# Optimization experiments

Hardware: AMD Instinct MI355X
Metric: run time of the kernel (lower is better)

The kernel has to match this reference:

```python
import jax, jax.numpy as jnp
import numpy as np

T, N, F = 32, 100000, 2
E = 1600000
H4 = 4 * F  # PyTorch LSTM packs gates i,f,g,o


def setup_inputs() -> dict:
    key = jax.random.key(0)
    ks = jax.random.split(key, 8)
    stdv = 1.0 / np.sqrt(F)
    x = jax.random.normal(ks[0], (T, N, F), dtype=jnp.float32)
    edge_index = jax.random.randint(ks[1], (2, E), 0, N, dtype=jnp.int32)
    mask = jax.random.randint(ks[2], (N,), 0, 2, dtype=jnp.int32).astype(bool)
    labels = jnp.zeros((N,), dtype=jnp.int32)
    edge_weight = jnp.ones((E,), dtype=jnp.float32)
    data = 0  # unused placeholder (pyg Data object in original)
    w_ih = jax.random.uniform(ks[3], (H4, F), minval=-stdv, maxval=stdv, dtype=jnp.float32)
    w_hh = jax.random.uniform(ks[4], (H4, F), minval=-stdv, maxval=stdv, dtype=jnp.float32)
    b_ih = jax.random.uniform(ks[5], (H4,), minval=-stdv, maxval=stdv, dtype=jnp.float32)
    b_hh = jax.random.uniform(ks[6], (H4,), minval=-stdv, maxval=stdv, dtype=jnp.float32)
    return {"x": x, "edge_index": edge_index, "mask": mask, "labels": labels,
            "edge_weight": edge_weight, "data": data,
            "w_ih": w_ih, "w_hh": w_hh, "b_ih": b_ih, "b_hh": b_hh}


def _interpolate(x, src, dst, n_nodes):
    # Iteratively fill zero entries with the mean over neighbors whose node
    # has any nonzero data (matches A[row_no_data,:]=0 edge filtering).
    def cond(carry):
        xx, i = carry
        return jnp.logical_and(jnp.any(xx == 0), i < 20)

    def body(carry):
        xx, i = carry
        has_data = jnp.sum(xx != 0, axis=(0, 2)) > 0            # [N]
        valid = has_data[src].astype(xx.dtype)                   # [E]
        msg = xx[:, src, :] * valid[None, :, None]               # [T,E,F]
        agg = jax.ops.segment_sum(jnp.transpose(msg, (1, 0, 2)), dst,
                                  num_segments=n_nodes)          # [N,T,F]
        cnt = jax.ops.segment_sum(valid, dst, num_segments=n_nodes)  # [N]
        mean = jnp.transpose(agg, (1, 0, 2)) / jnp.where(cnt > 0, cnt, 1.0)[None, :, None]
        return jnp.where(xx == 0, mean, xx), i + 1

    out, _ = jax.lax.while_loop(cond, body, (x, jnp.int32(0)))
    return out


def _lstm(x_seq, w_ih, w_hh, b_ih, b_hh):
    # x_seq: [T, N, F]; single-layer LSTM, hidden size F, gate order i,f,g,o.
    n, h = x_seq.shape[1], w_hh.shape[1]
    def step(carry, xt):
        hp, cp = carry
        g = xt @ w_ih.T + b_ih + hp @ w_hh.T + b_hh              # [N, 4F]
        i_, f_, g_, o_ = jnp.split(g, 4, axis=-1)
        i_ = jax.nn.sigmoid(i_); f_ = jax.nn.sigmoid(f_)
        g_ = jnp.tanh(g_);        o_ = jax.nn.sigmoid(o_)
        c = f_ * cp + i_ * g_
        hh = o_ * jnp.tanh(c)
        return (hh, c), hh
    z = jnp.zeros((n, h), dtype=x_seq.dtype)
    _, out = jax.lax.scan(step, (z, z), x_seq)
    return out


def reference(x, edge_index, mask, labels, edge_weight, data, w_ih, w_hh, b_ih, b_hh):
    masked = jnp.where(mask[None, :, None], x, jnp.zeros((), x.dtype))
    src, dst = edge_index[0], edge_index[1]
    interp_x = _interpolate(masked, src, dst, x.shape[1])
    return _lstm(interp_x, w_ih, w_hh, b_ih, b_hh)
```

## Files before the change

kernel.cpp:

```cpp
#include <hip/hip_runtime.h>
#include <math.h>

#define TT    32
#define NN    100000
#define FF    2
#define ROW   64
#define EE    1600000
#define MAXIT 20
#define LDSROW 66
#define BIGIT (1 << 29)
#define NR    8
#define RNG   (NN / NR)
#define SLOT  28
#define SLAB  (2 * SLOT)

typedef float f32x4 __attribute__((ext_vector_type(4)));
typedef float f32x2 __attribute__((ext_vector_type(2)));

__device__ __forceinline__ float fsig(float x) { return 1.0f / (1.0f + __expf(-x)); }
__device__ __forceinline__ float ftanh(float x) { return 2.0f / (1.0f + __expf(-2.0f * x)) - 1.0f; }

__global__ void k_mt_flags(const float* __restrict__ x, const int* __restrict__ mask,
                           float* __restrict__ xx, int* __restrict__ fill_iter,
                           unsigned char* __restrict__ hz, unsigned char* __restrict__ hd,
                           int* __restrict__ cnt_v, int* __restrict__ cnt_i,
                           int* __restrict__ wl_count) {
    __shared__ float tile[64 * LDSROW];
    const int n0 = blockIdx.x * 64;
    const int tid = threadIdx.x;

    if (tid < 64 && n0 + tid < NN) { cnt_v[n0 + tid] = 0; cnt_i[n0 + tid] = 0; }
    if (blockIdx.x == 0 && tid < 32) wl_count[tid] = 0;

#pragma unroll
    for (int r = 0; r < 16; r++) {
        int flat = r * 256 + tid;
        int t = flat >> 7;
        int col = flat & 127;
        int gcol = n0 * 2 + col;
        if (gcol < NN * FF) {
            int n = n0 + (col >> 1);
            float v = __builtin_nontemporal_load(x + (size_t)t * (NN * FF) + gcol);
            v = mask[n] ? v : 0.0f;
            tile[(col >> 1) * LDSROW + t * 2 + (col & 1)] = v;
        }
    }
    __syncthreads();

    const int lane = tid & 63, w = tid >> 6;
    for (int i = 0; i < 16; i++) {
        int ln = w * 16 + i;
        int n = n0 + ln;
        if (n >= NN) break;
        float v = tile[ln * LDSROW + lane];
        unsigned long long nzm = __ballot(v != 0.0f);
        if (lane == 0) {
            fill_iter[n] = (nzm != 0ull) ? 0 : BIGIT;
            hz[n] = (nzm != ~0ull) ? 1 : 0;
            hd[n] = (nzm != 0ull) ? 1 : 0;
        }
    }

#pragma unroll
    for (int j = 0; j < 4; j++) {
        int flat4 = j * 256 + tid;
        int ln = flat4 >> 4;
        int n = n0 + ln;
        if (n >= NN) continue;
        int off = (flat4 & 15) * 4;
        float4 v;
        v.x = tile[ln * LDSROW + off + 0];
        v.y = tile[ln * LDSROW + off + 1];
        v.z = tile[ln * LDSROW + off + 2];
        v.w = tile[ln * LDSROW + off + 3];
        *(float4*)(xx + (size_t)n * ROW + off) = v;
    }
}

__global__ void k_fill_slots(const int* __restrict__ ei, const unsigned char* __restrict__ hz,
                             const unsigned char* __restrict__ hd,
                             int* __restrict__ cnt_v, int* __restrict__ cnt_i,
                             int* __restrict__ slab) {
    const int r = blockIdx.x & (NR - 1);
    const int lo = r * RNG, hi = lo + RNG;
    const int gid = (blockIdx.x >> 3) * blockDim.x + threadIdx.x;
    const int stride = (gridDim.x >> 3) * blockDim.x;
    for (int e = gid; e < EE; e += stride) {
        int dst = ei[EE + e];
        if (dst < lo || dst >= hi) continue;
        if (!hz[dst]) continue;
        int src = ei[e];
        if (hd[src]) {
            int pos = atomicAdd(&cnt_v[dst], 1);
            if (pos < SLOT) slab[dst * SLAB + pos] = src;
        } else {
            int pos = atomicAdd(&cnt_i[dst], 1);
            if (pos < SLOT) slab[dst * SLAB + SLOT + pos] = src;
        }
    }
}

__device__ __forceinline__ void gather_node4(int n, int k, int lane,
                                             int vbeg, int vend, int ibeg, int iend,
                                             const int* __restrict__ slab,
                                             int* __restrict__ fill_iter,
                                             float* __restrict__ xx,
                                             int* __restrict__ wl_next,
                                             int* __restrict__ wl_count) {
    const int g = lane >> 4;
    const int s = lane & 15;
    float ax = 0.f, ay = 0.f, az = 0.f, aw = 0.f, cntv = 0.f;
#pragma unroll 2
    for (int e = vbeg + g; e < vend; e += 4) {
        int src = slab[e];
        f32x4 v = ((const f32x4*)(xx + (size_t)src * ROW))[s];
        ax += v.x; ay += v.y; az += v.z; aw += v.w; cntv += 1.f;
    }
    for (int e = ibeg + g; e < iend; e += 4) {
        int src = slab[e];
        if (fill_iter[src] < k) {
            f32x4 v = ((const f32x4*)(xx + (size_t)src * ROW))[s];
            ax += v.x; ay += v.y; az += v.z; aw += v.w; cntv += 1.f;
        }
    }
#pragma unroll
    for (int d = 16; d <= 32; d <<= 1) {
        ax += __shfl_xor(ax, d, 64);
        ay += __shfl_xor(ay, d, 64);
        az += __shfl_xor(az, d, 64);
        aw += __shfl_xor(aw, d, 64);
        cntv += __shfl_xor(cntv, d, 64);
    }
    f32x4 own = ((const f32x4*)(xx + (size_t)n * ROW))[s];
    bool has = cntv > 0.f;
    f32x4 nv;
    nv.x = (own.x == 0.f && has) ? ax / cntv : own.x;
    nv.y = (own.y == 0.f && has) ? ay / cntv : own.y;
    nv.z = (own.z == 0.f && has) ? az / cntv : own.z;
    nv.w = (own.w == 0.f && has) ? aw / cntv : own.w;
    bool allnz = (nv.x != 0.f) & (nv.y != 0.f) & (nv.z != 0.f) & (nv.w != 0.f);
    bool anynz = (nv.x != 0.f) | (nv.y != 0.f) | (nv.z != 0.f) | (nv.w != 0.f);
    unsigned long long ba = __ballot(allnz);
    unsigned long long bn = __ballot(anynz);
    if (g == 0) ((f32x4*)(xx + (size_t)n * ROW))[s] = nv;
    if (lane == 0) {
        if (bn != 0ull && fill_iter[n] > k) fill_iter[n] = k;
        if (ba != ~0ull) {
            int pos = atomicAdd(&wl_count[k], 1);
            wl_next[pos] = n;
        }
    }
}

__global__ void k_gather_first(const unsigned char* __restrict__ hz,
                               const int* __restrict__ cnt_v, const int* __restrict__ slab,
                               int* __restrict__ fill_iter, float* __restrict__ xx,
                               int* __restrict__ wl_next, int* __restrict__ wl_count) {
    const int lane = threadIdx.x & 63;
    int wave = (blockIdx.x * blockDim.x + threadIdx.x) >> 6;
    const int nwaves = (gridDim.x * blockDim.x) >> 6;
    for (int n0 = wave; n0 < NN; n0 += nwaves) {
        int n = __builtin_amdgcn_readfirstlane(n0);
        if (!hz[n]) continue;
        int cv = cnt_v[n]; if (cv > SLOT) cv = SLOT;
        gather_node4(n, 1, lane, n * SLAB, n * SLAB + cv, 0, 0,
                     slab, fill_iter, xx, wl_next, wl_count);
    }
}

__global__ __launch_bounds__(1024)
void k_gather_rest(int* __restrict__ wl_a, int* __restrict__ wl_b,
                   int* __restrict__ wl_count,
                   const int* __restrict__ cnt_v, const int* __restrict__ cnt_i,
                   const int* __restrict__ slab,
                   int* __restrict__ fill_iter, float* __restrict__ xx) {
    const int lane = threadIdx.x & 63;
    const int wave = threadIdx.x >> 6;
    for (int k = 2; k <= MAXIT; k++) {
        int cnt = atomicAdd(&wl_count[k - 1], 0);
        if (cnt == 0) break;
        int* prev = (k & 1) ? wl_b : wl_a;
        int* next = (k & 1) ? wl_a : wl_b;
        for (int w = wave; w < cnt; w += 16) {
            int n = __builtin_amdgcn_readfirstlane(prev[w]);
            int cv = cnt_v[n]; if (cv > SLOT) cv = SLOT;
            int ci = cnt_i[n]; if (ci > SLOT) ci = SLOT;
            gather_node4(n, k, lane, n * SLAB, n * SLAB + cv,
                         n * SLAB + SLOT, n * SLAB + SLOT + ci,
                         slab, fill_iter, xx, next, wl_count);
        }
        __threadfence();
        __syncthreads();
    }
}

__global__ void k_lstm(const float* __restrict__ xx,
                       const float* __restrict__ wih, const float* __restrict__ whh,
                       const float* __restrict__ bih, const float* __restrict__ bhh,
                       float* __restrict__ out) {
    int n = blockIdx.x * 64 + threadIdx.x;
    if (n >= NN) return;
    float Wi[8][2], Wh[8][2], B[8];
#pragma unroll
    for (int kk = 0; kk < 8; kk++) {
        Wi[kk][0] = wih[kk * 2]; Wi[kk][1] = wih[kk * 2 + 1];
        Wh[kk][0] = whh[kk * 2]; Wh[kk][1] = whh[kk * 2 + 1];
        B[kk] = bih[kk] + bhh[kk];
    }
    f32x4 r4[16];
    const f32x4* row4 = (const f32x4*)(xx + (size_t)n * ROW);
#pragma unroll
    for (int i = 0; i < 16; i++) r4[i] = __builtin_nontemporal_load(row4 + i);
    const float* row = (const float*)r4;

    float h0 = 0.f, h1 = 0.f, c0 = 0.f, c1 = 0.f;
#pragma unroll 4
    for (int t = 0; t < TT; t++) {
        float x0 = row[t * 2], x1 = row[t * 2 + 1];
        float g[8];
#pragma unroll
        for (int kk = 0; kk < 8; kk++)
            g[kk] = B[kk] + Wi[kk][0] * x0 + Wi[kk][1] * x1 + Wh[kk][0] * h0 + Wh[kk][1] * h1;
        float i0 = fsig(g[0]), i1 = fsig(g[1]);
        float f0 = fsig(g[2]), f1 = fsig(g[3]);
        float gg0 = ftanh(g[4]), gg1 = ftanh(g[5]);
        float o0 = fsig(g[6]), o1 = fsig(g[7]);
        c0 = f0 * c0 + i0 * gg0;
        c1 = f1 * c1 + i1 * gg1;
        h0 = o0 * ftanh(c0);
        h1 = o1 * ftanh(c1);
        *(float2*)(out + (size_t)t * (NN * FF) + n * 2) = make_float2(h0, h1);
    }
}

extern "C" void kernel_launch(void* const* d_in, const int* in_sizes, int n_in,
                              void* d_out, int out_size, void* d_ws, size_t ws_size,
                              hipStream_t stream) {
    const float* x    = (const float*)d_in[0];
    const int*   ei   = (const int*)d_in[1];
    const int*   mask = (const int*)d_in[2];
    const float* wih  = (const float*)d_in[6];
    const float* whh  = (const float*)d_in[7];
    const float* bih  = (const float*)d_in[8];
    const float* bhh  = (const float*)d_in[9];
    float* out = (float*)d_out;

    char* ws = (char*)d_ws;
    float* xx        = (float*)ws;
    int*   fill_iter = (int*)(ws + (size_t)NN * ROW * 4);
    int*   wl_count  = fill_iter + NN;
    unsigned char* hz = (unsigned char*)(wl_count + 32);
    unsigned char* hd = hz + ((NN + 15) & ~15);

    int* slab  = (int*)d_out;
    int* cnt_v = slab + NN * SLAB;
    int* cnt_i = cnt_v + NN;
    int* wl_a  = cnt_i + NN;
    int* wl_b  = wl_a + NN;

    k_mt_flags<<<(NN + 63) / 64, 256, 0, stream>>>(x, mask, xx, fill_iter, hz, hd,
                                                   cnt_v, cnt_i, wl_count);
    k_fill_slots<<<2048, 256, 0, stream>>>(ei, hz, hd, cnt_v, cnt_i, slab);
    k_gather_first<<<6250, 256, 0, stream>>>(hz, cnt_v, slab, fill_iter, xx, wl_a, wl_count);
    k_gather_rest<<<1, 1024, 0, stream>>>(wl_a, wl_b, wl_count, cnt_v, cnt_i, slab,
                                          fill_iter, xx);
    k_lstm<<<(NN + 63) / 64, 64, 0, stream>>>(xx, wih, whh, bih, bhh, out);
}
```

Before: 249.9 us.

## Compact filtered edges into per-range queues before building neighbor slabs

The single edge-scan kernel, in which each of eight blocks reads all edges and filters by destination range, is replaced by one compaction pass that reads the edge list once. It writes zero-destination edges into eight range-bucketed valid queues and one invalid queue, using block-local atomics for the offsets. A build kernel then fills the valid slabs from the compact queues. Invalid-source slabs are stored only for nodes with no valid neighbors, through a compact id map capped at 2048 entries, which shrinks slab memory. This adds two kernel launches and introduces capacity caps (QCAP, IQCAP, CIDCAP) that could silently drop edges on inputs with a different distribution.

```diff
diff --git a/kernel.cpp b/kernel.cpp
--- a/kernel.cpp
+++ b/kernel.cpp
@@ -12,10 +12,12 @@
 #define NR    8
 #define RNG   (NN / NR)
 #define SLOT  28
-#define SLAB  (2 * SLOT)
+#define QCAP   131072
+#define IQCAP  442368
+#define CIDCAP 2048
+#define CHUNK  782
 
 typedef float f32x4 __attribute__((ext_vector_type(4)));
-typedef float f32x2 __attribute__((ext_vector_type(2)));
 
 __device__ __forceinline__ float fsig(float x) { return 1.0f / (1.0f + __expf(-x)); }
 __device__ __forceinline__ float ftanh(float x) { return 2.0f / (1.0f + __expf(-2.0f * x)) - 1.0f; }
@@ -23,14 +25,19 @@
 __global__ void k_mt_flags(const float* __restrict__ x, const int* __restrict__ mask,
                            float* __restrict__ xx, int* __restrict__ fill_iter,
                            unsigned char* __restrict__ hz, unsigned char* __restrict__ hd,
-                           int* __restrict__ cnt_v, int* __restrict__ cnt_i,
+                           int* __restrict__ cnt_v, int* __restrict__ cidmap,
+                           int* __restrict__ icnt, int* __restrict__ qc,
                            int* __restrict__ wl_count) {
     __shared__ float tile[64 * LDSROW];
     const int n0 = blockIdx.x * 64;
     const int tid = threadIdx.x;
 
-    if (tid < 64 && n0 + tid < NN) { cnt_v[n0 + tid] = 0; cnt_i[n0 + tid] = 0; }
-    if (blockIdx.x == 0 && tid < 32) wl_count[tid] = 0;
+    if (tid < 64 && n0 + tid < NN) { cnt_v[n0 + tid] = 0; cidmap[n0 + tid] = 0; }
+    if (blockIdx.x == 0) {
+        if (tid < 32) wl_count[tid] = 0;
+        if (tid >= 64 && tid < 80) qc[tid - 64] = 0;
+    }
+    if (blockIdx.x < 8) icnt[blockIdx.x * 256 + tid] = 0;
 
 #pragma unroll
     for (int r = 0; r < 16; r++) {
@@ -77,32 +84,86 @@
     }
 }
 
-__global__ void k_fill_slots(const int* __restrict__ ei, const unsigned char* __restrict__ hz,
-                             const unsigned char* __restrict__ hd,
-                             int* __restrict__ cnt_v, int* __restrict__ cnt_i,
-                             int* __restrict__ slab) {
-    const int r = blockIdx.x & (NR - 1);
-    const int lo = r * RNG, hi = lo + RNG;
+__global__ void k_compact(const int* __restrict__ ei, const unsigned char* __restrict__ hz,
+                          const unsigned char* __restrict__ hd,
+                          int2* __restrict__ vq, int2* __restrict__ iq,
+                          int* __restrict__ qc) {
+    __shared__ int lcnt[9];
+    __shared__ int lbase[9];
+    const int tid = threadIdx.x;
+    if (tid < 9) lcnt[tid] = 0;
+    __syncthreads();
+    const int e0 = blockIdx.x * CHUNK;
+    const int e1 = min(e0 + CHUNK, EE);
+    int rs[4], rd[4], rb[4], rp[4];
+#pragma unroll
+    for (int i = 0; i < 4; i++) {
+        rb[i] = -1;
+        int e = e0 + i * 256 + tid;
+        if (e < e1) {
+            int dst = __builtin_nontemporal_load(ei + EE + e);
+            if (hz[dst]) {
+                int src = __builtin_nontemporal_load(ei + e);
+                int b = hd[src] ? (dst / RNG) : 8;
+                rs[i] = src; rd[i] = dst; rb[i] = b;
+                rp[i] = atomicAdd(&lcnt[b], 1);
+            }
+        }
+    }
+    __syncthreads();
+    if (tid < 9) lbase[tid] = atomicAdd(&qc[tid], lcnt[tid]);
+    __syncthreads();
+#pragma unroll
+    for (int i = 0; i < 4; i++) {
+        if (rb[i] >= 0) {
+            int b = rb[i];
+            int p = lbase[b] + rp[i];
+            if (b < 8) { if (p < QCAP)  vq[b * QCAP + p] = make_int2(rs[i], rd[i]); }
+            else       { if (p < IQCAP) iq[p]            = make_int2(rs[i], rd[i]); }
+        }
+    }
+}
+
+__global__ void k_build(const int2* __restrict__ vq, const int* __restrict__ qc,
+                        int* __restrict__ cnt_v, int* __restrict__ slab) {
+    const int r = blockIdx.x & 7;
+    int n = qc[r]; if (n > QCAP) n = QCAP;
     const int gid = (blockIdx.x >> 3) * blockDim.x + threadIdx.x;
     const int stride = (gridDim.x >> 3) * blockDim.x;
-    for (int e = gid; e < EE; e += stride) {
-        int dst = ei[EE + e];
-        if (dst < lo || dst >= hi) continue;
-        if (!hz[dst]) continue;
-        int src = ei[e];
-        if (hd[src]) {
-            int pos = atomicAdd(&cnt_v[dst], 1);
-            if (pos < SLOT) slab[dst * SLAB + pos] = src;
-        } else {
-            int pos = atomicAdd(&cnt_i[dst], 1);
-            if (pos < SLOT) slab[dst * SLAB + SLOT + pos] = src;
+    const int2* q = vq + r * QCAP;
+    for (int i = gid; i < n; i += stride) {
+        int2 sd = q[i];
+        int pos = atomicAdd(&cnt_v[sd.y], 1);
+        if (pos < SLOT) slab[sd.y * SLOT + pos] = sd.x;
+    }
+}
+
+__global__ void k_inv(const int2* __restrict__ iq, const int* __restrict__ qc,
+                      const int* __restrict__ cnt_v, int* __restrict__ cidmap,
+                      int* __restrict__ icnt, int* __restrict__ islab,
+                      int* __restrict__ ncid) {
+    int n = qc[8]; if (n > IQCAP) n = IQCAP;
+    const int gid = blockIdx.x * blockDim.x + threadIdx.x;
+    const int stride = gridDim.x * blockDim.x;
+    for (int i = gid; i < n; i += stride) {
+        int2 sd = iq[i];
+        if (cnt_v[sd.y] != 0) continue;
+        int cid = cidmap[sd.y];
+        if (cid == 0) {
+            int nid = atomicAdd(ncid, 1) + 1;
+            int old = atomicCAS(&cidmap[sd.y], 0, nid);
+            cid = old ? old : nid;
+        }
+        if (cid <= CIDCAP) {
+            int pos = atomicAdd(&icnt[cid - 1], 1);
+            if (pos < SLOT) islab[(cid - 1) * SLOT + pos] = sd.x;
         }
     }
 }
 
 __device__ __forceinline__ void gather_node4(int n, int k, int lane,
-                                             int vbeg, int vend, int ibeg, int iend,
-                                             const int* __restrict__ slab,
+                                             int vbeg, int vend, const int* __restrict__ vsl,
+                                             int ibeg, int iend, const int* __restrict__ isl,
                                              int* __restrict__ fill_iter,
                                              float* __restrict__ xx,
                                              int* __restrict__ wl_next,
@@ -112,12 +173,12 @@
     float ax = 0.f, ay = 0.f, az = 0.f, aw = 0.f, cntv = 0.f;
 #pragma unroll 2
     for (int e = vbeg + g; e < vend; e += 4) {
-        int src = slab[e];
+        int src = vsl[e];
         f32x4 v = ((const f32x4*)(xx + (size_t)src * ROW))[s];
         ax += v.x; ay += v.y; az += v.z; aw += v.w; cntv += 1.f;
     }
     for (int e = ibeg + g; e < iend; e += 4) {
-        int src = slab[e];
+        int src = isl[e];
         if (fill_iter[src] < k) {
             f32x4 v = ((const f32x4*)(xx + (size_t)src * ROW))[s];
             ax += v.x; ay += v.y; az += v.z; aw += v.w; cntv += 1.f;
@@ -163,15 +224,16 @@
         int n = __builtin_amdgcn_readfirstlane(n0);
         if (!hz[n]) continue;
         int cv = cnt_v[n]; if (cv > SLOT) cv = SLOT;
-        gather_node4(n, 1, lane, n * SLAB, n * SLAB + cv, 0, 0,
-                     slab, fill_iter, xx, wl_next, wl_count);
+        gather_node4(n, 1, lane, n * SLOT, n * SLOT + cv, slab, 0, 0, slab,
+                     fill_iter, xx, wl_next, wl_count);
     }
 }
 
 __global__ __launch_bounds__(1024)
 void k_gather_rest(int* __restrict__ wl_a, int* __restrict__ wl_b,
                    int* __restrict__ wl_count,
-                   const int* __restrict__ cnt_v, const int* __restrict__ cnt_i,
+                   const int* __restrict__ cnt_v, const int* __restrict__ cidmap,
+                   const int* __restrict__ icnt, const int* __restrict__ islab,
                    const int* __restrict__ slab,
                    int* __restrict__ fill_iter, float* __restrict__ xx) {
     const int lane = threadIdx.x & 63;
@@ -184,10 +246,15 @@
         for (int w = wave; w < cnt; w += 16) {
             int n = __builtin_amdgcn_readfirstlane(prev[w]);
             int cv = cnt_v[n]; if (cv > SLOT) cv = SLOT;
-            int ci = cnt_i[n]; if (ci > SLOT) ci = SLOT;
-            gather_node4(n, k, lane, n * SLAB, n * SLAB + cv,
-                         n * SLAB + SLOT, n * SLAB + SLOT + ci,
-                         slab, fill_iter, xx, next, wl_count);
+            int cid = cidmap[n];
+            int ci = 0, ib = 0;
+            if (cid > 0 && cid <= CIDCAP) {
+                ci = icnt[cid - 1]; if (ci > SLOT) ci = SLOT;
+                ib = (cid - 1) * SLOT;
+            }
+            gather_node4(n, k, lane, n * SLOT, n * SLOT + cv, slab,
+                         ib, ib + ci, islab,
+                         fill_iter, xx, next, wl_count);
         }
         __threadfence();
         __syncthreads();
@@ -252,17 +319,24 @@
     unsigned char* hz = (unsigned char*)(wl_count + 32);
     unsigned char* hd = hz + ((NN + 15) & ~15);
 
-    int* slab  = (int*)d_out;
-    int* cnt_v = slab + NN * SLAB;
-    int* cnt_i = cnt_v + NN;
-    int* wl_a  = cnt_i + NN;
-    int* wl_b  = wl_a + NN;
+    int*  slab   = (int*)d_out;
+    int2* vq     = (int2*)(slab + (size_t)NN * SLOT);
+    int2* iq     = vq + 8 * (size_t)QCAP;
+    int*  cnt_v  = (int*)(iq + IQCAP);
+    int*  cidmap = cnt_v + NN;
+    int*  wl_a   = cidmap + NN;
+    int*  wl_b   = wl_a + NN;
+    int*  icnt   = wl_b + NN;
+    int*  islab  = icnt + CIDCAP;
+    int*  qc     = islab + CIDCAP * SLOT;
 
     k_mt_flags<<<(NN + 63) / 64, 256, 0, stream>>>(x, mask, xx, fill_iter, hz, hd,
-                                                   cnt_v, cnt_i, wl_count);
-    k_fill_slots<<<2048, 256, 0, stream>>>(ei, hz, hd, cnt_v, cnt_i, slab);
+                                                   cnt_v, cidmap, icnt, qc, wl_count);
+    k_compact<<<(EE + CHUNK - 1) / CHUNK, 256, 0, stream>>>(ei, hz, hd, vq, iq, qc);
+    k_build<<<2048, 256, 0, stream>>>(vq, qc, cnt_v, slab);
+    k_inv<<<512, 256, 0, stream>>>(iq, qc, cnt_v, cidmap, icnt, islab, qc + 9);
     k_gather_first<<<6250, 256, 0, stream>>>(hz, cnt_v, slab, fill_iter, xx, wl_a, wl_count);
-    k_gather_rest<<<1, 1024, 0, stream>>>(wl_a, wl_b, wl_count, cnt_v, cnt_i, slab,
-                                          fill_iter, xx);
+    k_gather_rest<<<1, 1024, 0, stream>>>(wl_a, wl_b, wl_count, cnt_v, cidmap, icnt, islab,
+                                          slab, fill_iter, xx);
     k_lstm<<<(NN + 63) / 64, 64, 0, stream>>>(xx, wih, whh, bih, bhh, out);
 }
```

Result: slower. 256.7 us (+2.7%).
